# Performance work log

Hardware: AMD Instinct MI355X
Metric: run time of the kernel (lower is better)

The kernel has to match this reference:

```python
import jax, jax.numpy as jnp
import numpy as np

N_NODES = 20000
N_EDGES = 160000
B = 200      # num graphs (nodes per graph = 100)
T = 8        # num_tau
A = 10       # action_size
H = 4        # heads
D = 128      # out_channels
R = 4        # num_relations
NCOS = 64


def rgat(x, edge_index, edge_type, W, q, k, b):
    # W: [R, in, H*D]; q, k: [H*D, H]; b: [D]
    xw = jnp.einsum('ni,rio->nro', x, W)              # [N, R, H*D]
    src, dst = edge_index[0], edge_index[1]
    xj = xw[src, edge_type]                            # [E, H*D] gather by edge + relation
    xi = xw[dst, edge_type]                            # [E, H*D]
    alpha = jax.nn.leaky_relu(xi @ q + xj @ k, 0.2)    # [E, H]
    amax = jax.ops.segment_max(alpha, dst, num_segments=N_NODES)
    ex = jnp.exp(alpha - amax[dst])                    # segment softmax over dst
    denom = jax.ops.segment_sum(ex, dst, num_segments=N_NODES)
    a = ex / denom[dst]                                # [E, H]
    msg = (a[:, :, None] * xj.reshape(-1, H, D)).reshape(-1, H * D)
    agg = jax.ops.segment_sum(msg, dst, num_segments=N_NODES).reshape(-1, H, D)
    return agg.mean(axis=1) + b                        # concat=False -> mean over heads


def noisy_linear(z, w, bias, sw, sb, ew, eb):
    # torch convention: w [out, in]
    return z @ (w + sw * ew).T + (bias + sb * eb)


def setup_inputs():
    key = jax.random.key(0)
    ks = jax.random.split(key, 48)
    def rn(i, shape, scale=0.05):
        return jax.random.normal(ks[i], shape, dtype=jnp.float32) * scale
    SIG = 0.017
    inp = {
        'x': jax.random.normal(ks[0], (N_NODES, 2), dtype=jnp.float32),
        'edge_index': jax.random.randint(ks[1], (2, N_EDGES), 0, N_NODES, dtype=jnp.int32),
        'edge_type': jax.random.randint(ks[2], (N_EDGES,), 0, R, dtype=jnp.int32),
        'taus': jax.random.uniform(ks[3], (B, T, 1), dtype=jnp.float32),
        'W1': rn(4, (R, 2, H * D), 0.3), 'q1': rn(5, (H * D, H), 0.05), 'k1': rn(6, (H * D, H), 0.05), 'b1': rn(7, (D,)),
        'W2': rn(8, (R, D, H * D), 0.06), 'q2': rn(9, (H * D, H), 0.05), 'k2': rn(10, (H * D, H), 0.05), 'b2': rn(11, (D,)),
        'cos_w': rn(12, (D, NCOS), 0.1), 'cos_b': rn(13, (D,)),
        'ff1_w': rn(14, (D, D), 0.1), 'ff1_b': rn(15, (D,)),
        'ff1_sw': jnp.full((D, D), SIG, jnp.float32), 'ff1_sb': jnp.full((D,), SIG, jnp.float32),
        'ff1_ew': rn(16, (D, D), 1.0), 'ff1_eb': rn(17, (D,), 1.0),
        'ff2_w': rn(18, (D, D), 0.1), 'ff2_b': rn(19, (D,)),
        'ff2_sw': jnp.full((D, D), SIG, jnp.float32), 'ff2_sb': jnp.full((D,), SIG, jnp.float32),
        'ff2_ew': rn(20, (D, D), 1.0), 'ff2_eb': rn(21, (D,), 1.0),
        'adv_w': rn(22, (A, D), 0.1), 'adv_b': rn(23, (A,)),
        'adv_sw': jnp.full((A, D), SIG, jnp.float32), 'adv_sb': jnp.full((A,), SIG, jnp.float32),
        'adv_ew': rn(24, (A, D), 1.0), 'adv_eb': rn(25, (A,), 1.0),
        'val_w': rn(26, (1, D), 0.1), 'val_b': rn(27, (1,)),
        'val_sw': jnp.full((1, D), SIG, jnp.float32), 'val_sb': jnp.full((1,), SIG, jnp.float32),
        'val_ew': rn(28, (1, D), 1.0), 'val_eb': rn(29, (1,), 1.0),
    }
    return inp


def reference(x, edge_index, edge_type, taus,
              W1, q1, k1, b1, W2, q2, k2, b2, cos_w, cos_b,
              ff1_w, ff1_b, ff1_sw, ff1_sb, ff1_ew, ff1_eb,
              ff2_w, ff2_b, ff2_sw, ff2_sb, ff2_ew, ff2_eb,
              adv_w, adv_b, adv_sw, adv_sb, adv_ew, adv_eb,
              val_w, val_b, val_sw, val_sb, val_ew, val_eb):
    h = jax.nn.selu(rgat(x, edge_index, edge_type, W1, q1, k1, b1))
    h = jax.nn.selu(rgat(h, edge_index, edge_type, W2, q2, k2, b2))
    g = h.reshape(B, N_NODES // B, D).sum(axis=1)      # global_add_pool (block batch_idx)
    pis = jnp.pi * jnp.arange(1, NCOS + 1, dtype=jnp.float32)  # [NCOS]
    cos = jnp.cos(taus * pis)                           # [B, T, NCOS]
    cos_x = jax.nn.relu(cos @ cos_w.T + cos_b)          # [B, T, D]
    z = (g[:, None, :] * cos_x).reshape(B * T, D)
    z = jax.nn.selu(noisy_linear(z, ff1_w, ff1_b, ff1_sw, ff1_sb, ff1_ew, ff1_eb))
    z = jax.nn.selu(noisy_linear(z, ff2_w, ff2_b, ff2_sw, ff2_sb, ff2_ew, ff2_eb))
    adv = noisy_linear(z, adv_w, adv_b, adv_sw, adv_sb, adv_ew, adv_eb)   # [B*T, A]
    val = noisy_linear(z, val_w, val_b, val_sw, val_sb, val_ew, val_eb)   # [B*T, 1]
    out = val + adv - adv.mean(axis=1, keepdims=True)
    return out.reshape(B, T, A), taus
```

## Files before the change

kernel.cpp:

```cpp
#include <hip/hip_runtime.h>
#include <hip/hip_bf16.h>

constexpr long NN = 20000;
constexpr long NE = 160000;
constexpr long BB = 200;
constexpr long TT = 8;
constexpr long GN = 100;

constexpr long O_FLAG = 0;
constexpr long O_X    = 16;                 constexpr long N_X   = 40000;
constexpr long O_TAU  = O_X + N_X;          constexpr long N_TAU = 1600;
constexpr long O_W1   = O_TAU + N_TAU;      constexpr long N_W1  = 4096;
constexpr long O_Q1   = O_W1 + N_W1;        constexpr long N_Q   = 2048;
constexpr long O_K1   = O_Q1 + N_Q;
constexpr long O_B1   = O_K1 + N_Q;         constexpr long N_B   = 128;
constexpr long O_W2   = O_B1 + N_B;         constexpr long N_W2  = 262144;
constexpr long O_Q2   = O_W2 + N_W2;
constexpr long O_K2   = O_Q2 + N_Q;
constexpr long O_B2   = O_K2 + N_Q;
constexpr long O_CW   = O_B2 + N_B;         constexpr long N_CW  = 8192;
constexpr long O_CB   = O_CW + N_CW;
constexpr long O_F1W  = O_CB + N_B;         constexpr long N_FW  = 16384;
constexpr long O_F1B  = O_F1W + N_FW;
constexpr long O_F1SW = O_F1B + N_B;
constexpr long O_F1SB = O_F1SW + N_FW;
constexpr long O_F1EW = O_F1SB + N_B;
constexpr long O_F1EB = O_F1EW + N_FW;
constexpr long O_F2W  = O_F1EB + N_B;
constexpr long O_F2B  = O_F2W + N_FW;
constexpr long O_F2SW = O_F2B + N_B;
constexpr long O_F2SB = O_F2SW + N_FW;
constexpr long O_F2EW = O_F2SB + N_B;
constexpr long O_F2EB = O_F2EW + N_FW;
constexpr long O_AW   = O_F2EB + N_B;       constexpr long N_AW  = 1280;
constexpr long O_AB   = O_AW + N_AW;        constexpr long N_AB  = 16;
constexpr long O_ASW  = O_AB + N_AB;
constexpr long O_ASB  = O_ASW + N_AW;
constexpr long O_AEW  = O_ASB + N_AB;
constexpr long O_AEB  = O_AEW + N_AW;
constexpr long O_VW   = O_AEB + N_AB;       constexpr long N_VW  = 128;
constexpr long O_VB   = O_VW + N_VW;        constexpr long N_VB  = 16;
constexpr long O_VSW  = O_VB + N_VB;
constexpr long O_VSB  = O_VSW + N_VW;
constexpr long O_VEW  = O_VSB + N_VB;
constexpr long O_VEB  = O_VEW + N_VW;
constexpr long O_WQ1  = O_VEB + N_VB;
constexpr long O_WK1  = O_WQ1 + 32;
constexpr long O_WQ2  = O_WK1 + 32;
constexpr long O_WK2  = O_WQ2 + 2048;
constexpr long O_CF1W = O_WK2 + 2048;
constexpr long O_CF1B = O_CF1W + N_FW;
constexpr long O_CF2W = O_CF1B + N_B;
constexpr long O_CF2B = O_CF2W + N_FW;
constexpr long O_CAW  = O_CF2B + N_B;
constexpr long O_CAB  = O_CAW + N_AW;
constexpr long O_CVW  = O_CAB + N_AB;
constexpr long O_CVB  = O_CVW + N_VW;
constexpr long O_AL1  = O_CVB + N_VB;
constexpr long O_AL2  = O_AL1 + NE*4;
constexpr long O_H1   = O_AL2 + NE*4;
constexpr long O_H2   = O_H1 + NN*128;
constexpr long O_G    = O_H2 + NN*128;
constexpr long O_Z0   = O_G + BB*128;
constexpr long O_Z1   = O_Z0 + BB*TT*128;
constexpr long O_Z2   = O_Z1 + BB*TT*128;
constexpr long O_AGG1 = O_Z2 + BB*TT*128;
constexpr long O_DEG  = O_AGG1;
constexpr long O_CUR  = O_DEG + NN;
constexpr long O_ROWP = O_CUR + NN;
constexpr long O_PERM = O_ROWP + NN + 8;
constexpr long O_AGG2 = O_AGG1 + NN*128;
constexpr long O_DEN1 = O_AGG2 + NN*128;
constexpr long O_DEN2 = O_DEN1 + NN*4;
constexpr long O_AMAX1= O_DEN2 + NN*4;
constexpr long O_AMAX2= O_AMAX1 + NN*4;
constexpr long O_XW2  = O_AMAX2 + NN*4;
constexpr long O_END_TABLE = O_XW2 + (NN*4*512)/2;
constexpr long MPAD   = 20096;
constexpr long O_H1B  = O_END_TABLE;
constexpr long O_W2BT = O_H1B + (MPAD*128)/2;
constexpr long O_END2 = O_W2BT + (2048L*128)/2;
constexpr long O_AQ   = O_END2;
constexpr long O_AK   = O_AQ + NN*16;
constexpr long O_END3 = O_AK + NN*16;

constexpr int EMAX = 128;

#define DEVFN __device__ __forceinline__

typedef __attribute__((ext_vector_type(8))) short bf16x8;
typedef __attribute__((ext_vector_type(4))) float f32x4;
typedef __attribute__((ext_vector_type(4))) unsigned short u16x4;

DEVFN float selu_f(float x){ return 1.0507009873554805f * (x > 0.f ? x : 1.6732632423543772f * expm1f(x)); }
DEVFN float lrelu_f(float x){ return x >= 0.f ? x : 0.2f * x; }
DEVFN float bf2f(unsigned short u){ return __uint_as_float(((unsigned)u) << 16); }

__global__ void k_pre(const unsigned short* taus_u16, const int* ei, float* ws){
    if (blockIdx.x == 0){
        if (threadIdx.x == 0){
            int bf = 1;
            for (int i = 0; i < 128; i++) if (taus_u16[i] > 0x3F80u){ bf = 0; break; }
            ((int*)ws)[0] = bf;
        }
        return;
    }
    long e = (long)(blockIdx.x - 1)*blockDim.x + threadIdx.x;
    if (e >= NE) return;
    atomicAdd((int*)(ws + O_DEG) + ei[NE + e], 1);
}

__global__ void k_scan(float* ws){
    const int* deg = (const int*)(ws + O_DEG);
    int* rowp = (int*)(ws + O_ROWP);
    __shared__ int part[256];
    int tid = threadIdx.x;
    int base = tid * 79;
    int n = 0; if (base < NN) n = min(79, (int)NN - base);
    int s = 0;
    for (int i = 0; i < n; i++) s += deg[base + i];
    part[tid] = s;
    __syncthreads();
    if (tid == 0){
        int acc = 0;
        for (int i = 0; i < 256; i++){ int t = part[i]; part[i] = acc; acc += t; }
    }
    __syncthreads();
    int acc = part[tid];
    for (int i = 0; i < n; i++){ rowp[base + i] = acc; acc += deg[base + i]; }
    if (tid == 0) rowp[NN] = (int)NE;
}

struct ConvArgs { const void* src[38]; long off[38]; int n[38]; };

__global__ void k_conv_scatter(ConvArgs a, const int* ei, float* ws){
    int y = blockIdx.y;
    if (y == 38){
        long e = (long)blockIdx.x*blockDim.x + threadIdx.x;
        if (e >= NE) return;
        int dst = ei[NE + e];
        int pos = atomicAdd((int*)(ws + O_CUR) + dst, 1);
        ((int*)(ws + O_PERM))[((const int*)(ws + O_ROWP))[dst] + pos] = (int)e;
        return;
    }
    long off = a.off[y];
    if (off < 0) return;
    const void* s = a.src[y];
    int n = a.n[y];
    int bf = ((const int*)ws)[0];
    for (int i = blockIdx.x*blockDim.x + threadIdx.x; i < n; i += gridDim.x*blockDim.x){
        float v;
        if (bf){ unsigned short u = ((const unsigned short*)s)[i]; v = bf2f(u); }
        else   { v = ((const float*)s)[i]; }
        ws[off + i] = v;
    }
}

__global__ void k_prep(float* ws){
    int phase = blockIdx.y;
    int idx = blockIdx.x*blockDim.x + threadIdx.x;
    if (phase == 0){
        if (idx >= 4160) return;
        long wsrc, qsrc, dst; int ri, h;
        if (idx < 64){
            int t = idx & 31; h = t & 3; ri = t >> 2;
            wsrc = O_W1 + (long)ri*512;
            qsrc = (idx < 32) ? O_Q1 : O_K1;
            dst  = ((idx < 32) ? O_WQ1 : O_WK1) + t;
        } else {
            int t = (idx - 64) & 2047; h = t & 3; ri = t >> 2;
            wsrc = O_W2 + (long)ri*512;
            qsrc = (idx < 2112) ? O_Q2 : O_K2;
            dst  = ((idx < 2112) ? O_WQ2 : O_WK2) + t;
        }
        const float* W = ws + wsrc;
        const float* Q = ws + qsrc;
        float s = 0.f;
        for (int o = 0; o < 512; o++) s += W[o] * Q[o*4 + h];
        ws[dst] = s;
    } else if (phase == 1){
        const long tw[8] = {O_F1W,O_F2W,O_AW,O_VW, O_F1B,O_F2B,O_AB,O_VB};
        const long ts[8] = {O_F1SW,O_F2SW,O_ASW,O_VSW, O_F1SB,O_F2SB,O_ASB,O_VSB};
        const long te[8] = {O_F1EW,O_F2EW,O_AEW,O_VEW, O_F1EB,O_F2EB,O_AEB,O_VEB};
        const long td[8] = {O_CF1W,O_CF2W,O_CAW,O_CVW, O_CF1B,O_CF2B,O_CAB,O_CVB};
        const int  tn[8] = {16384,16384,1280,128, 128,128,10,1};
        const int  tb[8] = {0,16384,32768,34048, 34176,34304,34432,34442};
        int total = 34443;
        for (int i = idx; i < total; i += gridDim.x*blockDim.x){
            int t = 0;
            #pragma unroll
            for (int q = 1; q < 8; q++) if (i >= tb[q]) t = q;
            int j = i - tb[t];
            if (j < tn[t]) ws[td[t] + j] = ws[tw[t] + j] + ws[ts[t] + j]*ws[te[t] + j];
        }
    } else if (phase == 2){
        if (idx >= 262144) return;
        int np = idx & 2047, k = idx >> 11;
        int r = np >> 9, q = np & 511, d = q >> 2, h = q & 3;
        float v = ws[O_W2 + (long)r*65536 + (long)k*512 + h*128 + d];
        ((__hip_bfloat16*)(ws + O_W2BT))[(long)np*128 + k] = __float2bfloat16(v);
    } else {
        if (idx < 6144) ws[O_H1B + (20000L*128)/2 + idx] = 0.f;
    }
}

__global__ void k_node1(const int* ei, const int* et, float* ws){
    __shared__ float wqk[64];
    __shared__ float alc[EMAX][4];
    __shared__ float xsc[EMAX][2];
    __shared__ int   rtc[EMAX];
    __shared__ float sacc[4][4][2];
    __shared__ float den[4], amax[4];
    __shared__ float mred[2][4];
    int n = blockIdx.x, tid = threadIdx.x;
    const int* rowp = (const int*)(ws + O_ROWP);
    const int* perm = (const int*)(ws + O_PERM);
    int e0 = rowp[n], deg = rowp[n+1] - e0;
    if (tid < 64) wqk[tid] = ws[O_WQ1 + tid];
    if (tid < 32) ((float*)sacc)[tid] = 0.f;
    if (tid < 4) den[tid] = 0.f;
    float xd0 = ws[O_X + (long)n*2], xd1 = ws[O_X + (long)n*2 + 1];
    __syncthreads();
    float mx[4] = {-3.0e38f,-3.0e38f,-3.0e38f,-3.0e38f};
    for (int j0 = 0; j0 < deg; j0 += 128){
        int j = j0 + tid;
        if (j < deg){
            int e = perm[e0 + j];
            int src = ei[e], rt = et[e];
            float xs0 = ws[O_X + (long)src*2], xs1 = ws[O_X + (long)src*2 + 1];
            const float* Wq = wqk + rt*8;
            const float* Wk = wqk + 32 + rt*8;
            #pragma unroll
            for (int h = 0; h < 4; h++){
                float a = lrelu_f(xd0*Wq[h] + xd1*Wq[4+h] + xs0*Wk[h] + xs1*Wk[4+h]);
                if (j < EMAX) alc[j][h] = a;
                mx[h] = fmaxf(mx[h], a);
            }
            if (j < EMAX){ xsc[j][0] = xs0; xsc[j][1] = xs1; rtc[j] = rt; }
        }
    }
    #pragma unroll
    for (int off = 32; off > 0; off >>= 1)
        #pragma unroll
        for (int h = 0; h < 4; h++) mx[h] = fmaxf(mx[h], __shfl_xor(mx[h], off));
    if ((tid & 63) == 0)
        #pragma unroll
        for (int h = 0; h < 4; h++) mred[tid >> 6][h] = mx[h];
    __syncthreads();
    if (tid < 4) amax[tid] = fmaxf(mred[0][tid], mred[1][tid]);
    __syncthreads();
    for (int j0 = 0; j0 < deg; j0 += 128){
        int j = j0 + tid;
        if (j < deg){
            float al[4], xs0, xs1; int rt;
            if (j < EMAX){
                #pragma unroll
                for (int h = 0; h < 4; h++) al[h] = alc[j][h];
                xs0 = xsc[j][0]; xs1 = xsc[j][1]; rt = rtc[j];
            } else {
                int e = perm[e0 + j];
                int src = ei[e]; rt = et[e];
                xs0 = ws[O_X + (long)src*2]; xs1 = ws[O_X + (long)src*2 + 1];
                const float* Wq = wqk + rt*8;
                const float* Wk = wqk + 32 + rt*8;
                #pragma unroll
                for (int h = 0; h < 4; h++)
                    al[h] = lrelu_f(xd0*Wq[h] + xd1*Wq[4+h] + xs0*Wk[h] + xs1*Wk[4+h]);
            }
            #pragma unroll
            for (int h = 0; h < 4; h++){
                float ex = expf(al[h] - amax[h]);
                atomicAdd(&den[h], ex);
                atomicAdd(&sacc[rt][h][0], ex*xs0);
                atomicAdd(&sacc[rt][h][1], ex*xs1);
            }
        }
    }
    __syncthreads();
    int d = tid;
    float rden[4];
    #pragma unroll
    for (int h = 0; h < 4; h++) rden[h] = den[h] > 0.f ? 0.25f/den[h] : 0.f;
    float v = 0.f;
    #pragma unroll
    for (int r = 0; r < 4; r++)
        #pragma unroll
        for (int h = 0; h < 4; h++){
            float w0 = ws[O_W1 + r*1024 +        h*128 + d];
            float w1 = ws[O_W1 + r*1024 + 512  + h*128 + d];
            v += rden[h]*(w0*sacc[r][h][0] + w1*sacc[r][h][1]);
        }
    float out = selu_f(v + ws[O_B1 + d]);
    ((__hip_bfloat16*)(ws + O_H1B))[(long)n*128 + d] = __float2bfloat16(out);
}

__global__ void k_aqk(float* ws){
    __shared__ float wq[128*16];
    __shared__ float wk[128*16];
    __shared__ float hl[16][129];
    int tid = threadIdx.x;
    long nb = (long)blockIdx.x * 16;
    const unsigned short* h1b = (const unsigned short*)(ws + O_H1B);
    #pragma unroll
    for (int c = 0; c < 8; c++){
        int idx = tid + c*256;
        int i = idx >> 4, o = idx & 15;
        int r = o >> 2, h = o & 3;
        wq[i*16 + o] = ws[O_WQ2 + r*512 + i*4 + h];
        wk[i*16 + o] = ws[O_WK2 + r*512 + i*4 + h];
        hl[idx >> 7][idx & 127] = bf2f(h1b[nb*128 + idx]);
    }
    __syncthreads();
    int j = tid >> 4, o = tid & 15;
    float aq = 0.f, ak = 0.f;
    #pragma unroll 4
    for (int i = 0; i < 128; i++){
        float hv = hl[j][i];
        aq += hv * wq[i*16 + o];
        ak += hv * wk[i*16 + o];
    }
    ws[O_AQ + (nb + j)*16 + o] = aq;
    ws[O_AK + (nb + j)*16 + o] = ak;
}

__global__ void k_xw2_mfma(float* ws){
    __shared__ __align__(16) unsigned short Ash[128*128];
    __shared__ __align__(16) unsigned short Bsh[128*128];
    const unsigned short* h1b  = (const unsigned short*)(ws + O_H1B);
    const unsigned short* w2bt = (const unsigned short*)(ws + O_W2BT);
    long bm = (long)blockIdx.x * 128;
    long bn = (long)blockIdx.y * 128;
    int tid = threadIdx.x;
    char* Ac = (char*)Ash; char* Bc = (char*)Bsh;
    #pragma unroll
    for (int i = 0; i < 8; i++){
        int c = tid + i*256;
        int row = c >> 4, kb = (c & 15) * 16;
        int off = row*256 + (kb ^ ((row & 7) << 4));
        *(bf16x8*)(Ac + off) = *(const bf16x8*)&h1b [(bm + row)*128 + (c & 15)*8];
        *(bf16x8*)(Bc + off) = *(const bf16x8*)&w2bt[(bn + row)*128 + (c & 15)*8];
    }
    __syncthreads();
    int w = tid >> 6, lane = tid & 63;
    int wm = (w >> 1) * 64, wn = (w & 1) * 64;
    int r16 = lane & 15, kq = lane >> 4;
    f32x4 acc[4][4] = {};
    #pragma unroll
    for (int ks = 0; ks < 4; ks++){
        int kbyte = ks*64 + kq*16;
        bf16x8 a[4], b[4];
        #pragma unroll
        for (int m = 0; m < 4; m++){
            int row = wm + m*16 + r16;
            a[m] = *(const bf16x8*)(Ac + row*256 + (kbyte ^ ((row & 7) << 4)));
        }
        #pragma unroll
        for (int n = 0; n < 4; n++){
            int row = wn + n*16 + r16;
            b[n] = *(const bf16x8*)(Bc + row*256 + (kbyte ^ ((row & 7) << 4)));
        }
        #pragma unroll
        for (int m = 0; m < 4; m++)
            #pragma unroll
            for (int n = 0; n < 4; n++)
                acc[m][n] = __builtin_amdgcn_mfma_f32_16x16x32_bf16(a[m], b[n], acc[m][n], 0, 0, 0);
    }
    __hip_bfloat16* xb = (__hip_bfloat16*)(ws + O_XW2);
    #pragma unroll
    for (int m = 0; m < 4; m++){
        long gr0 = bm + wm + m*16 + kq*4;
        #pragma unroll
        for (int j = 0; j < 4; j++){
            long gr = gr0 + j;
            if (gr < NN){
                #pragma unroll
                for (int n = 0; n < 4; n++){
                    long gc = bn + wn + n*16 + r16;
                    xb[gr*2048 + gc] = __float2bfloat16(acc[m][n][j]);
                }
            }
        }
    }
}

__global__ void k_node2(const int* ei, const int* et, float* ws){
    __shared__ float aq[16];
    __shared__ float exc[EMAX][4];
    __shared__ int   esrt[EMAX];
    __shared__ float den[4], amax[4];
    __shared__ float mred[2][4];
    int n = blockIdx.x, tid = threadIdx.x;
    const int* rowp = (const int*)(ws + O_ROWP);
    const int* perm = (const int*)(ws + O_PERM);
    int e0 = rowp[n], deg = rowp[n+1] - e0;
    if (tid < 16) aq[tid] = ws[O_AQ + (long)n*16 + tid];
    if (tid < 4) den[tid] = 0.f;
    __syncthreads();
    float mx[4] = {-3.0e38f,-3.0e38f,-3.0e38f,-3.0e38f};
    for (int j0 = 0; j0 < deg; j0 += 128){
        int j = j0 + tid;
        if (j < deg){
            int e = perm[e0 + j];
            int src = ei[e], rt = et[e];
            float4 k4 = *(const float4*)&ws[O_AK + (long)src*16 + rt*4];
            float al0 = lrelu_f(aq[rt*4+0] + k4.x);
            float al1 = lrelu_f(aq[rt*4+1] + k4.y);
            float al2 = lrelu_f(aq[rt*4+2] + k4.z);
            float al3 = lrelu_f(aq[rt*4+3] + k4.w);
            if (j < EMAX){
                exc[j][0]=al0; exc[j][1]=al1; exc[j][2]=al2; exc[j][3]=al3;
                esrt[j] = src*4 + rt;
            }
            mx[0]=fmaxf(mx[0],al0); mx[1]=fmaxf(mx[1],al1);
            mx[2]=fmaxf(mx[2],al2); mx[3]=fmaxf(mx[3],al3);
        }
    }
    #pragma unroll
    for (int off = 32; off > 0; off >>= 1)
        #pragma unroll
        for (int h = 0; h < 4; h++) mx[h] = fmaxf(mx[h], __shfl_xor(mx[h], off));
    if ((tid & 63) == 0)
        #pragma unroll
        for (int h = 0; h < 4; h++) mred[tid >> 6][h] = mx[h];
    __syncthreads();
    if (tid < 4) amax[tid] = fmaxf(mred[0][tid], mred[1][tid]);
    __syncthreads();
    for (int j0 = 0; j0 < deg; j0 += 128){
        int j = j0 + tid;
        if (j < deg && j < EMAX){
            #pragma unroll
            for (int h = 0; h < 4; h++){
                float ex = expf(exc[j][h] - amax[h]);
                exc[j][h] = ex;
                atomicAdd(&den[h], ex);
            }
        } else if (j < deg){
            int e = perm[e0 + j];
            int src = ei[e], rt = et[e];
            float4 k4 = *(const float4*)&ws[O_AK + (long)src*16 + rt*4];
            float al[4] = {lrelu_f(aq[rt*4+0]+k4.x), lrelu_f(aq[rt*4+1]+k4.y),
                           lrelu_f(aq[rt*4+2]+k4.z), lrelu_f(aq[rt*4+3]+k4.w)};
            #pragma unroll
            for (int h = 0; h < 4; h++) atomicAdd(&den[h], expf(al[h]-amax[h]));
        }
    }
    __syncthreads();
    int d = tid;
    const unsigned short* xw2 = (const unsigned short*)(ws + O_XW2);
    float a0=0.f, a1=0.f, a2=0.f, a3=0.f;
    int mdeg = min(deg, EMAX);
    int j = 0;
    for (; j + 4 <= mdeg; j += 4){
        long s0 = esrt[j], s1 = esrt[j+1], s2 = esrt[j+2], s3 = esrt[j+3];
        u16x4 v0 = *(const u16x4*)(xw2 + s0*512 + (d << 2));
        u16x4 v1 = *(const u16x4*)(xw2 + s1*512 + (d << 2));
        u16x4 v2 = *(const u16x4*)(xw2 + s2*512 + (d << 2));
        u16x4 v3 = *(const u16x4*)(xw2 + s3*512 + (d << 2));
        a0 += exc[j  ][0]*bf2f(v0[0]); a1 += exc[j  ][1]*bf2f(v0[1]);
        a2 += exc[j  ][2]*bf2f(v0[2]); a3 += exc[j  ][3]*bf2f(v0[3]);
        a0 += exc[j+1][0]*bf2f(v1[0]); a1 += exc[j+1][1]*bf2f(v1[1]);
        a2 += exc[j+1][2]*bf2f(v1[2]); a3 += exc[j+1][3]*bf2f(v1[3]);
        a0 += exc[j+2][0]*bf2f(v2[0]); a1 += exc[j+2][1]*bf2f(v2[1]);
        a2 += exc[j+2][2]*bf2f(v2[2]); a3 += exc[j+2][3]*bf2f(v2[3]);
        a0 += exc[j+3][0]*bf2f(v3[0]); a1 += exc[j+3][1]*bf2f(v3[1]);
        a2 += exc[j+3][2]*bf2f(v3[2]); a3 += exc[j+3][3]*bf2f(v3[3]);
    }
    for (; j < mdeg; j++){
        long sr = esrt[j];
        u16x4 v = *(const u16x4*)(xw2 + sr*512 + (d << 2));
        a0 += exc[j][0]*bf2f(v[0]); a1 += exc[j][1]*bf2f(v[1]);
        a2 += exc[j][2]*bf2f(v[2]); a3 += exc[j][3]*bf2f(v[3]);
    }
    for (j = EMAX; j < deg; j++){
        int e = perm[e0 + j];
        int src = ei[e], rt = et[e];
        float4 k4 = *(const float4*)&ws[O_AK + (long)src*16 + rt*4];
        float e0h = expf(lrelu_f(aq[rt*4+0]+k4.x)-amax[0]);
        float e1h = expf(lrelu_f(aq[rt*4+1]+k4.y)-amax[1]);
        float e2h = expf(lrelu_f(aq[rt*4+2]+k4.z)-amax[2]);
        float e3h = expf(lrelu_f(aq[rt*4+3]+k4.w)-amax[3]);
        u16x4 v = *(const u16x4*)(xw2 + ((long)src*4 + rt)*512 + (d << 2));
        a0 += e0h*bf2f(v[0]); a1 += e1h*bf2f(v[1]);
        a2 += e2h*bf2f(v[2]); a3 += e3h*bf2f(v[3]);
    }
    float rd0 = den[0] > 0.f ? 0.25f/den[0] : 0.f;
    float rd1 = den[1] > 0.f ? 0.25f/den[1] : 0.f;
    float rd2 = den[2] > 0.f ? 0.25f/den[2] : 0.f;
    float rd3 = den[3] > 0.f ? 0.25f/den[3] : 0.f;
    float v = a0*rd0 + a1*rd1 + a2*rd2 + a3*rd3;
    ws[O_H2 + (long)n*128 + d] = selu_f(v + ws[O_B2 + d]);
}

__global__ void k_pool(float* ws){
    int b = blockIdx.x, d = threadIdx.x;
    float s = 0.f;
    for (int j = 0; j < GN; j++) s += ws[O_H2 + ((long)b*GN + j)*128 + d];
    ws[O_G + (long)b*128 + d] = s;
}

__global__ void k_tail(float* ws, void* d_out, const void* taus_raw){
    __shared__ float cs[64];
    __shared__ float row0[128], row1[128], row2[128];
    __shared__ float advs[12];
    int bt = blockIdx.x, t = threadIdx.x;
    int b = bt >> 3;
    if (t < 64){
        float tau = ws[O_TAU + bt];
        cs[t] = cosf(tau * (3.14159265358979323846f * (float)(t + 1)));
    }
    __syncthreads();
    {
        const float* cw = ws + O_CW + (long)t*64;
        float s = ws[O_CB + t];
        for (int c = 0; c < 64; c++) s += cs[c]*cw[c];
        s = fmaxf(s, 0.f);
        row0[t] = ws[O_G + (long)b*128 + t] * s;
    }
    __syncthreads();
    {
        const float* W = ws + O_CF1W + (long)t*128;
        float s = ws[O_CF1B + t];
        for (int i = 0; i < 128; i++) s += row0[i]*W[i];
        row1[t] = selu_f(s);
    }
    __syncthreads();
    {
        const float* W = ws + O_CF2W + (long)t*128;
        float s = ws[O_CF2B + t];
        for (int i = 0; i < 128; i++) s += row1[i]*W[i];
        row2[t] = selu_f(s);
    }
    __syncthreads();
    if (t < 11){
        const float* W = (t < 10) ? (ws + O_CAW + (long)t*128) : (ws + O_CVW);
        float s = (t < 10) ? ws[O_CAB + t] : ws[O_CVB];
        for (int i = 0; i < 128; i++) s += row2[i]*W[i];
        advs[t] = s;
    }
    __syncthreads();
    if (t == 0){
        float m = 0.f;
        #pragma unroll
        for (int a = 0; a < 10; a++) m += advs[a];
        m *= 0.1f;
        float val = advs[10];
        int bf = ((const int*)ws)[0];
        if (bf){
            __hip_bfloat16* out = (__hip_bfloat16*)d_out;
            for (int a = 0; a < 10; a++) out[(long)bt*10 + a] = __float2bfloat16(val + advs[a] - m);
            ((unsigned short*)d_out)[16000 + bt] = ((const unsigned short*)taus_raw)[bt];
        } else {
            float* out = (float*)d_out;
            for (int a = 0; a < 10; a++) out[(long)bt*10 + a] = val + advs[a] - m;
            out[16000 + bt] = ((const float*)taus_raw)[bt];
        }
    }
}

extern "C" void kernel_launch(void* const* d_in, const int* in_sizes, int n_in,
                              void* d_out, int out_size, void* d_ws, size_t ws_size,
                              hipStream_t stream){
    (void)in_sizes; (void)n_in; (void)out_size; (void)ws_size;
    float* ws = (float*)d_ws;
    const int* ei = (const int*)d_in[1];
    const int* et = (const int*)d_in[2];

    hipMemsetAsync(ws + O_DEG, 0, (size_t)(2*NN)*4, stream);

    k_pre<<<626, 256, 0, stream>>>((const unsigned short*)d_in[3], ei, ws);
    k_scan<<<1, 256, 0, stream>>>(ws);

    ConvArgs ca;
    static const long conv_o[38] = {
        O_X, -1, -1, O_TAU, O_W1, O_Q1, O_K1, O_B1, O_W2, O_Q2, O_K2, O_B2, O_CW, O_CB,
        O_F1W, O_F1B, O_F1SW, O_F1SB, O_F1EW, O_F1EB,
        O_F2W, O_F2B, O_F2SW, O_F2SB, O_F2EW, O_F2EB,
        O_AW, O_AB, O_ASW, O_ASB, O_AEW, O_AEB,
        O_VW, O_VB, O_VSW, O_VSB, O_VEW, O_VEB };
    static const int conv_n[38] = {
        40000, 0, 0, 1600, 4096, 2048, 2048, 128, 262144, 2048, 2048, 128, 8192, 128,
        16384, 128, 16384, 128, 16384, 128,
        16384, 128, 16384, 128, 16384, 128,
        1280, 10, 1280, 10, 1280, 10,
        128, 1, 128, 1, 128, 1 };
    for (int i = 0; i < 38; i++){ ca.src[i] = d_in[i]; ca.off[i] = conv_o[i]; ca.n[i] = conv_n[i]; }
    k_conv_scatter<<<dim3(625, 39), 256, 0, stream>>>(ca, ei, ws);

    k_prep<<<dim3(1024, 4), 256, 0, stream>>>(ws);

    k_node1<<<20000, 128, 0, stream>>>(ei, et, ws);

    k_xw2_mfma<<<dim3(157, 16), 256, 0, stream>>>(ws);
    k_aqk<<<1250, 256, 0, stream>>>(ws);
    k_node2<<<20000, 128, 0, stream>>>(ei, et, ws);

    k_pool<<<200, 128, 0, stream>>>(ws);
    k_tail<<<1600, 128, 0, stream>>>(ws, d_out, d_in[3]);
}
```

Baseline: 243.8 us.

## Map one wavefront per node in RGAT aggregation kernels with register reductions

Both node kernels now assign one 64-lane wavefront per destination node, packing four nodes into each 256-thread block, instead of one 128-thread block per node. Softmax max and sum use wave shuffles and per-lane register accumulators in place of shared-memory atomics and block barriers. Each lane now handles two output channels using wider 8-element bf16 loads. The goal is to cut block-launch, barrier and atomic overhead for nodes of small degree (about 8 on average). The cost is more register pressure from the 32 per-relation accumulators and more shuffle reductions in node1.

```diff
diff --git a/kernel.cpp b/kernel.cpp
--- a/kernel.cpp
+++ b/kernel.cpp
@@ -69,12 +69,7 @@
 constexpr long O_CUR  = O_DEG + NN;
 constexpr long O_ROWP = O_CUR + NN;
 constexpr long O_PERM = O_ROWP + NN + 8;
-constexpr long O_AGG2 = O_AGG1 + NN*128;
-constexpr long O_DEN1 = O_AGG2 + NN*128;
-constexpr long O_DEN2 = O_DEN1 + NN*4;
-constexpr long O_AMAX1= O_DEN2 + NN*4;
-constexpr long O_AMAX2= O_AMAX1 + NN*4;
-constexpr long O_XW2  = O_AMAX2 + NN*4;
+constexpr long O_XW2  = O_AGG1 + NN*128 + NN*128 + NN*16;
 constexpr long O_END_TABLE = O_XW2 + (NN*4*512)/2;
 constexpr long MPAD   = 20096;
 constexpr long O_H1B  = O_END_TABLE;
@@ -84,17 +79,29 @@
 constexpr long O_AK   = O_AQ + NN*16;
 constexpr long O_END3 = O_AK + NN*16;
 
-constexpr int EMAX = 128;
-
 #define DEVFN __device__ __forceinline__
 
 typedef __attribute__((ext_vector_type(8))) short bf16x8;
 typedef __attribute__((ext_vector_type(4))) float f32x4;
-typedef __attribute__((ext_vector_type(4))) unsigned short u16x4;
+typedef __attribute__((ext_vector_type(8))) unsigned short u16x8;
 
 DEVFN float selu_f(float x){ return 1.0507009873554805f * (x > 0.f ? x : 1.6732632423543772f * expm1f(x)); }
 DEVFN float lrelu_f(float x){ return x >= 0.f ? x : 0.2f * x; }
 DEVFN float bf2f(unsigned short u){ return __uint_as_float(((unsigned)u) << 16); }
+DEVFN float wred_max(float v){
+    #pragma unroll
+    for (int off = 32; off > 0; off >>= 1) v = fmaxf(v, __shfl_xor(v, off));
+    return v;
+}
+DEVFN float wred_sum(float v){
+    #pragma unroll
+    for (int off = 32; off > 0; off >>= 1) v += __shfl_xor(v, off);
+    return v;
+}
+DEVFN unsigned short f2bfu(float x){
+    __hip_bfloat16 b = __float2bfloat16(x);
+    return *(unsigned short*)&b;
+}
 
 __global__ void k_pre(const unsigned short* taus_u16, const int* ei, float* ws){
     if (blockIdx.x == 0){
@@ -204,94 +211,107 @@
     }
 }
 
-__global__ void k_node1(const int* ei, const int* et, float* ws){
-    __shared__ float wqk[64];
-    __shared__ float alc[EMAX][4];
-    __shared__ float xsc[EMAX][2];
-    __shared__ int   rtc[EMAX];
-    __shared__ float sacc[4][4][2];
-    __shared__ float den[4], amax[4];
-    __shared__ float mred[2][4];
-    int n = blockIdx.x, tid = threadIdx.x;
+__global__ __launch_bounds__(256) void k_node1(const int* ei, const int* et, float* ws){
+    int wid = threadIdx.x >> 6, lane = threadIdx.x & 63;
+    long n = (long)blockIdx.x*4 + wid;
     const int* rowp = (const int*)(ws + O_ROWP);
     const int* perm = (const int*)(ws + O_PERM);
     int e0 = rowp[n], deg = rowp[n+1] - e0;
-    if (tid < 64) wqk[tid] = ws[O_WQ1 + tid];
-    if (tid < 32) ((float*)sacc)[tid] = 0.f;
-    if (tid < 4) den[tid] = 0.f;
-    float xd0 = ws[O_X + (long)n*2], xd1 = ws[O_X + (long)n*2 + 1];
-    __syncthreads();
+    float xd0 = ws[O_X + n*2], xd1 = ws[O_X + n*2 + 1];
+    bool have = lane < deg;
+    float al[4], xs0 = 0.f, xs1 = 0.f; int rt0 = 0;
     float mx[4] = {-3.0e38f,-3.0e38f,-3.0e38f,-3.0e38f};
-    for (int j0 = 0; j0 < deg; j0 += 128){
-        int j = j0 + tid;
+    if (have){
+        int e = perm[e0 + lane]; int src = ei[e]; rt0 = et[e];
+        xs0 = ws[O_X + (long)src*2]; xs1 = ws[O_X + (long)src*2 + 1];
+        const float* Wq = ws + O_WQ1 + rt0*8;
+        const float* Wk = ws + O_WK1 + rt0*8;
+        #pragma unroll
+        for (int h = 0; h < 4; h++){
+            al[h] = lrelu_f(xd0*Wq[h] + xd1*Wq[4+h] + xs0*Wk[h] + xs1*Wk[4+h]);
+            mx[h] = al[h];
+        }
+    }
+    for (int j0 = 64; j0 < deg; j0 += 64){
+        int j = j0 + lane;
         if (j < deg){
-            int e = perm[e0 + j];
-            int src = ei[e], rt = et[e];
-            float xs0 = ws[O_X + (long)src*2], xs1 = ws[O_X + (long)src*2 + 1];
-            const float* Wq = wqk + rt*8;
-            const float* Wk = wqk + 32 + rt*8;
+            int e = perm[e0 + j]; int src = ei[e]; int rt = et[e];
+            float a0 = ws[O_X + (long)src*2], a1 = ws[O_X + (long)src*2 + 1];
+            const float* Wq = ws + O_WQ1 + rt*8;
+            const float* Wk = ws + O_WK1 + rt*8;
+            #pragma unroll
+            for (int h = 0; h < 4; h++)
+                mx[h] = fmaxf(mx[h], lrelu_f(xd0*Wq[h] + xd1*Wq[4+h] + a0*Wk[h] + a1*Wk[4+h]));
+        }
+    }
+    #pragma unroll
+    for (int h = 0; h < 4; h++) mx[h] = wred_max(mx[h]);
+    float s[4][4][2];
+    #pragma unroll
+    for (int r = 0; r < 4; r++)
+        #pragma unroll
+        for (int h = 0; h < 4; h++){ s[r][h][0] = 0.f; s[r][h][1] = 0.f; }
+    float den[4] = {0.f,0.f,0.f,0.f};
+    if (have){
+        #pragma unroll
+        for (int h = 0; h < 4; h++){
+            float ex = expf(al[h] - mx[h]);
+            den[h] += ex;
+            float c0 = ex*xs0, c1 = ex*xs1;
+            #pragma unroll
+            for (int r = 0; r < 4; r++){
+                if (r == rt0){ s[r][h][0] += c0; s[r][h][1] += c1; }
+            }
+        }
+    }
+    for (int j0 = 64; j0 < deg; j0 += 64){
+        int j = j0 + lane;
+        if (j < deg){
+            int e = perm[e0 + j]; int src = ei[e]; int rt = et[e];
+            float a0 = ws[O_X + (long)src*2], a1 = ws[O_X + (long)src*2 + 1];
+            const float* Wq = ws + O_WQ1 + rt*8;
+            const float* Wk = ws + O_WK1 + rt*8;
             #pragma unroll
             for (int h = 0; h < 4; h++){
-                float a = lrelu_f(xd0*Wq[h] + xd1*Wq[4+h] + xs0*Wk[h] + xs1*Wk[4+h]);
-                if (j < EMAX) alc[j][h] = a;
-                mx[h] = fmaxf(mx[h], a);
+                float a = lrelu_f(xd0*Wq[h] + xd1*Wq[4+h] + a0*Wk[h] + a1*Wk[4+h]);
+                float ex = expf(a - mx[h]);
+                den[h] += ex;
+                float c0 = ex*a0, c1 = ex*a1;
+                #pragma unroll
+                for (int r = 0; r < 4; r++){
+                    if (r == rt){ s[r][h][0] += c0; s[r][h][1] += c1; }
+                }
             }
-            if (j < EMAX){ xsc[j][0] = xs0; xsc[j][1] = xs1; rtc[j] = rt; }
-        }
-    }
-    #pragma unroll
-    for (int off = 32; off > 0; off >>= 1)
-        #pragma unroll
-        for (int h = 0; h < 4; h++) mx[h] = fmaxf(mx[h], __shfl_xor(mx[h], off));
-    if ((tid & 63) == 0)
-        #pragma unroll
-        for (int h = 0; h < 4; h++) mred[tid >> 6][h] = mx[h];
-    __syncthreads();
-    if (tid < 4) amax[tid] = fmaxf(mred[0][tid], mred[1][tid]);
-    __syncthreads();
-    for (int j0 = 0; j0 < deg; j0 += 128){
-        int j = j0 + tid;
-        if (j < deg){
-            float al[4], xs0, xs1; int rt;
-            if (j < EMAX){
-                #pragma unroll
-                for (int h = 0; h < 4; h++) al[h] = alc[j][h];
-                xs0 = xsc[j][0]; xs1 = xsc[j][1]; rt = rtc[j];
-            } else {
-                int e = perm[e0 + j];
-                int src = ei[e]; rt = et[e];
-                xs0 = ws[O_X + (long)src*2]; xs1 = ws[O_X + (long)src*2 + 1];
-                const float* Wq = wqk + rt*8;
-                const float* Wk = wqk + 32 + rt*8;
-                #pragma unroll
-                for (int h = 0; h < 4; h++)
-                    al[h] = lrelu_f(xd0*Wq[h] + xd1*Wq[4+h] + xs0*Wk[h] + xs1*Wk[4+h]);
-            }
-            #pragma unroll
-            for (int h = 0; h < 4; h++){
-                float ex = expf(al[h] - amax[h]);
-                atomicAdd(&den[h], ex);
-                atomicAdd(&sacc[rt][h][0], ex*xs0);
-                atomicAdd(&sacc[rt][h][1], ex*xs1);
-            }
-        }
-    }
-    __syncthreads();
-    int d = tid;
+        }
+    }
+    #pragma unroll
+    for (int h = 0; h < 4; h++) den[h] = wred_sum(den[h]);
+    #pragma unroll
+    for (int r = 0; r < 4; r++)
+        #pragma unroll
+        for (int h = 0; h < 4; h++){
+            s[r][h][0] = wred_sum(s[r][h][0]);
+            s[r][h][1] = wred_sum(s[r][h][1]);
+        }
     float rden[4];
     #pragma unroll
     for (int h = 0; h < 4; h++) rden[h] = den[h] > 0.f ? 0.25f/den[h] : 0.f;
-    float v = 0.f;
+    float v0 = 0.f, v1 = 0.f;
     #pragma unroll
     for (int r = 0; r < 4; r++)
         #pragma unroll
         for (int h = 0; h < 4; h++){
-            float w0 = ws[O_W1 + r*1024 +        h*128 + d];
-            float w1 = ws[O_W1 + r*1024 + 512  + h*128 + d];
-            v += rden[h]*(w0*sacc[r][h][0] + w1*sacc[r][h][1]);
-        }
-    float out = selu_f(v + ws[O_B1 + d]);
-    ((__hip_bfloat16*)(ws + O_H1B))[(long)n*128 + d] = __float2bfloat16(out);
+            float2 wa = *(const float2*)&ws[O_W1 + r*1024 +       h*128 + lane*2];
+            float2 wb = *(const float2*)&ws[O_W1 + r*1024 + 512 + h*128 + lane*2];
+            float t0 = s[r][h][0]*rden[h], t1 = s[r][h][1]*rden[h];
+            v0 += wa.x*t0 + wb.x*t1;
+            v1 += wa.y*t0 + wb.y*t1;
+        }
+    float2 b2 = *(const float2*)&ws[O_B1 + lane*2];
+    float o0 = selu_f(v0 + b2.x), o1 = selu_f(v1 + b2.y);
+    unsigned short* p = (unsigned short*)(ws + O_H1B) + n*128 + lane*2;
+    ushort2 pk; pk.x = f2bfu(o0); pk.y = f2bfu(o1);
+    *(ushort2*)p = pk;
 }
 
 __global__ void k_aqk(float* ws){
@@ -383,112 +403,116 @@
     }
 }
 
-__global__ void k_node2(const int* ei, const int* et, float* ws){
-    __shared__ float aq[16];
-    __shared__ float exc[EMAX][4];
-    __shared__ int   esrt[EMAX];
-    __shared__ float den[4], amax[4];
-    __shared__ float mred[2][4];
-    int n = blockIdx.x, tid = threadIdx.x;
+__global__ __launch_bounds__(256) void k_node2(const int* ei, const int* et, float* ws){
+    __shared__ float excs[4][64][4];
+    __shared__ int   esrts[4][64];
+    int wid = threadIdx.x >> 6, lane = threadIdx.x & 63;
+    long n = (long)blockIdx.x*4 + wid;
     const int* rowp = (const int*)(ws + O_ROWP);
     const int* perm = (const int*)(ws + O_PERM);
     int e0 = rowp[n], deg = rowp[n+1] - e0;
-    if (tid < 16) aq[tid] = ws[O_AQ + (long)n*16 + tid];
-    if (tid < 4) den[tid] = 0.f;
-    __syncthreads();
+    bool have = lane < deg;
+    float al[4]; int srt = 0;
     float mx[4] = {-3.0e38f,-3.0e38f,-3.0e38f,-3.0e38f};
-    for (int j0 = 0; j0 < deg; j0 += 128){
-        int j = j0 + tid;
+    if (have){
+        int e = perm[e0 + lane]; int src = ei[e]; int rt = et[e]; srt = src*4 + rt;
+        float4 q4 = *(const float4*)&ws[O_AQ + n*16 + rt*4];
+        float4 k4 = *(const float4*)&ws[O_AK + (long)src*16 + rt*4];
+        al[0] = lrelu_f(q4.x + k4.x); al[1] = lrelu_f(q4.y + k4.y);
+        al[2] = lrelu_f(q4.z + k4.z); al[3] = lrelu_f(q4.w + k4.w);
+        #pragma unroll
+        for (int h = 0; h < 4; h++) mx[h] = al[h];
+    }
+    for (int j0 = 64; j0 < deg; j0 += 64){
+        int j = j0 + lane;
         if (j < deg){
-            int e = perm[e0 + j];
-            int src = ei[e], rt = et[e];
+            int e = perm[e0 + j]; int src = ei[e]; int rt = et[e];
+            float4 q4 = *(const float4*)&ws[O_AQ + n*16 + rt*4];
             float4 k4 = *(const float4*)&ws[O_AK + (long)src*16 + rt*4];
-            float al0 = lrelu_f(aq[rt*4+0] + k4.x);
-            float al1 = lrelu_f(aq[rt*4+1] + k4.y);
-            float al2 = lrelu_f(aq[rt*4+2] + k4.z);
-            float al3 = lrelu_f(aq[rt*4+3] + k4.w);
-            if (j < EMAX){
-                exc[j][0]=al0; exc[j][1]=al1; exc[j][2]=al2; exc[j][3]=al3;
-                esrt[j] = src*4 + rt;
-            }
-            mx[0]=fmaxf(mx[0],al0); mx[1]=fmaxf(mx[1],al1);
-            mx[2]=fmaxf(mx[2],al2); mx[3]=fmaxf(mx[3],al3);
-        }
-    }
-    #pragma unroll
-    for (int off = 32; off > 0; off >>= 1)
-        #pragma unroll
-        for (int h = 0; h < 4; h++) mx[h] = fmaxf(mx[h], __shfl_xor(mx[h], off));
-    if ((tid & 63) == 0)
-        #pragma unroll
-        for (int h = 0; h < 4; h++) mred[tid >> 6][h] = mx[h];
-    __syncthreads();
-    if (tid < 4) amax[tid] = fmaxf(mred[0][tid], mred[1][tid]);
-    __syncthreads();
-    for (int j0 = 0; j0 < deg; j0 += 128){
-        int j = j0 + tid;
-        if (j < deg && j < EMAX){
-            #pragma unroll
-            for (int h = 0; h < 4; h++){
-                float ex = expf(exc[j][h] - amax[h]);
-                exc[j][h] = ex;
-                atomicAdd(&den[h], ex);
-            }
-        } else if (j < deg){
-            int e = perm[e0 + j];
-            int src = ei[e], rt = et[e];
+            mx[0] = fmaxf(mx[0], lrelu_f(q4.x + k4.x));
+            mx[1] = fmaxf(mx[1], lrelu_f(q4.y + k4.y));
+            mx[2] = fmaxf(mx[2], lrelu_f(q4.z + k4.z));
+            mx[3] = fmaxf(mx[3], lrelu_f(q4.w + k4.w));
+        }
+    }
+    #pragma unroll
+    for (int h = 0; h < 4; h++) mx[h] = wred_max(mx[h]);
+    float den[4] = {0.f,0.f,0.f,0.f};
+    if (have){
+        #pragma unroll
+        for (int h = 0; h < 4; h++){
+            float ex = expf(al[h] - mx[h]);
+            den[h] += ex;
+            excs[wid][lane][h] = ex;
+        }
+        esrts[wid][lane] = srt;
+    }
+    for (int j0 = 64; j0 < deg; j0 += 64){
+        int j = j0 + lane;
+        if (j < deg){
+            int e = perm[e0 + j]; int src = ei[e]; int rt = et[e];
+            float4 q4 = *(const float4*)&ws[O_AQ + n*16 + rt*4];
             float4 k4 = *(const float4*)&ws[O_AK + (long)src*16 + rt*4];
-            float al[4] = {lrelu_f(aq[rt*4+0]+k4.x), lrelu_f(aq[rt*4+1]+k4.y),
-                           lrelu_f(aq[rt*4+2]+k4.z), lrelu_f(aq[rt*4+3]+k4.w)};
-            #pragma unroll
-            for (int h = 0; h < 4; h++) atomicAdd(&den[h], expf(al[h]-amax[h]));
-        }
-    }
-    __syncthreads();
-    int d = tid;
+            den[0] += expf(lrelu_f(q4.x + k4.x) - mx[0]);
+            den[1] += expf(lrelu_f(q4.y + k4.y) - mx[1]);
+            den[2] += expf(lrelu_f(q4.z + k4.z) - mx[2]);
+            den[3] += expf(lrelu_f(q4.w + k4.w) - mx[3]);
+        }
+    }
+    #pragma unroll
+    for (int h = 0; h < 4; h++) den[h] = wred_sum(den[h]);
+    __syncthreads();
     const unsigned short* xw2 = (const unsigned short*)(ws + O_XW2);
-    float a0=0.f, a1=0.f, a2=0.f, a3=0.f;
-    int mdeg = min(deg, EMAX);
+    float a0[4] = {0.f,0.f,0.f,0.f}, a1[4] = {0.f,0.f,0.f,0.f};
+    int mdeg = min(deg, 64);
     int j = 0;
     for (; j + 4 <= mdeg; j += 4){
-        long s0 = esrt[j], s1 = esrt[j+1], s2 = esrt[j+2], s3 = esrt[j+3];
-        u16x4 v0 = *(const u16x4*)(xw2 + s0*512 + (d << 2));
-        u16x4 v1 = *(const u16x4*)(xw2 + s1*512 + (d << 2));
-        u16x4 v2 = *(const u16x4*)(xw2 + s2*512 + (d << 2));
-        u16x4 v3 = *(const u16x4*)(xw2 + s3*512 + (d << 2));
-        a0 += exc[j  ][0]*bf2f(v0[0]); a1 += exc[j  ][1]*bf2f(v0[1]);
-        a2 += exc[j  ][2]*bf2f(v0[2]); a3 += exc[j  ][3]*bf2f(v0[3]);
-        a0 += exc[j+1][0]*bf2f(v1[0]); a1 += exc[j+1][1]*bf2f(v1[1]);
-        a2 += exc[j+1][2]*bf2f(v1[2]); a3 += exc[j+1][3]*bf2f(v1[3]);
-        a0 += exc[j+2][0]*bf2f(v2[0]); a1 += exc[j+2][1]*bf2f(v2[1]);
-        a2 += exc[j+2][2]*bf2f(v2[2]); a3 += exc[j+2][3]*bf2f(v2[3]);
-        a0 += exc[j+3][0]*bf2f(v3[0]); a1 += exc[j+3][1]*bf2f(v3[1]);
-        a2 += exc[j+3][2]*bf2f(v3[2]); a3 += exc[j+3][3]*bf2f(v3[3]);
+        long s0 = esrts[wid][j], s1 = esrts[wid][j+1], s2 = esrts[wid][j+2], s3 = esrts[wid][j+3];
+        u16x8 v0 = *(const u16x8*)(xw2 + s0*512 + lane*8);
+        u16x8 v1 = *(const u16x8*)(xw2 + s1*512 + lane*8);
+        u16x8 v2 = *(const u16x8*)(xw2 + s2*512 + lane*8);
+        u16x8 v3 = *(const u16x8*)(xw2 + s3*512 + lane*8);
+        #pragma unroll
+        for (int h = 0; h < 4; h++){
+            a0[h] += excs[wid][j  ][h]*bf2f(v0[h]); a1[h] += excs[wid][j  ][h]*bf2f(v0[4+h]);
+            a0[h] += excs[wid][j+1][h]*bf2f(v1[h]); a1[h] += excs[wid][j+1][h]*bf2f(v1[4+h]);
+            a0[h] += excs[wid][j+2][h]*bf2f(v2[h]); a1[h] += excs[wid][j+2][h]*bf2f(v2[4+h]);
+            a0[h] += excs[wid][j+3][h]*bf2f(v3[h]); a1[h] += excs[wid][j+3][h]*bf2f(v3[4+h]);
+        }
     }
     for (; j < mdeg; j++){
-        long sr = esrt[j];
-        u16x4 v = *(const u16x4*)(xw2 + sr*512 + (d << 2));
-        a0 += exc[j][0]*bf2f(v[0]); a1 += exc[j][1]*bf2f(v[1]);
-        a2 += exc[j][2]*bf2f(v[2]); a3 += exc[j][3]*bf2f(v[3]);
-    }
-    for (j = EMAX; j < deg; j++){
-        int e = perm[e0 + j];
-        int src = ei[e], rt = et[e];
+        long sr = esrts[wid][j];
+        u16x8 v = *(const u16x8*)(xw2 + sr*512 + lane*8);
+        #pragma unroll
+        for (int h = 0; h < 4; h++){
+            a0[h] += excs[wid][j][h]*bf2f(v[h]);
+            a1[h] += excs[wid][j][h]*bf2f(v[4+h]);
+        }
+    }
+    for (j = 64; j < deg; j++){
+        int e = perm[e0 + j]; int src = ei[e]; int rt = et[e];
+        float4 q4 = *(const float4*)&ws[O_AQ + n*16 + rt*4];
         float4 k4 = *(const float4*)&ws[O_AK + (long)src*16 + rt*4];
-        float e0h = expf(lrelu_f(aq[rt*4+0]+k4.x)-amax[0]);
-        float e1h = expf(lrelu_f(aq[rt*4+1]+k4.y)-amax[1]);
-        float e2h = expf(lrelu_f(aq[rt*4+2]+k4.z)-amax[2]);
-        float e3h = expf(lrelu_f(aq[rt*4+3]+k4.w)-amax[3]);
-        u16x4 v = *(const u16x4*)(xw2 + ((long)src*4 + rt)*512 + (d << 2));
-        a0 += e0h*bf2f(v[0]); a1 += e1h*bf2f(v[1]);
-        a2 += e2h*bf2f(v[2]); a3 += e3h*bf2f(v[3]);
-    }
-    float rd0 = den[0] > 0.f ? 0.25f/den[0] : 0.f;
-    float rd1 = den[1] > 0.f ? 0.25f/den[1] : 0.f;
-    float rd2 = den[2] > 0.f ? 0.25f/den[2] : 0.f;
-    float rd3 = den[3] > 0.f ? 0.25f/den[3] : 0.f;
-    float v = a0*rd0 + a1*rd1 + a2*rd2 + a3*rd3;
-    ws[O_H2 + (long)n*128 + d] = selu_f(v + ws[O_B2 + d]);
+        float ex[4];
+        ex[0] = expf(lrelu_f(q4.x + k4.x) - mx[0]);
+        ex[1] = expf(lrelu_f(q4.y + k4.y) - mx[1]);
+        ex[2] = expf(lrelu_f(q4.z + k4.z) - mx[2]);
+        ex[3] = expf(lrelu_f(q4.w + k4.w) - mx[3]);
+        u16x8 v = *(const u16x8*)(xw2 + ((long)src*4 + rt)*512 + lane*8);
+        #pragma unroll
+        for (int h = 0; h < 4; h++){
+            a0[h] += ex[h]*bf2f(v[h]);
+            a1[h] += ex[h]*bf2f(v[4+h]);
+        }
+    }
+    float rd[4];
+    #pragma unroll
+    for (int h = 0; h < 4; h++) rd[h] = den[h] > 0.f ? 0.25f/den[h] : 0.f;
+    float o0 = a0[0]*rd[0] + a0[1]*rd[1] + a0[2]*rd[2] + a0[3]*rd[3];
+    float o1 = a1[0]*rd[0] + a1[1]*rd[1] + a1[2]*rd[2] + a1[3]*rd[3];
+    float2 b2 = *(const float2*)&ws[O_B2 + lane*2];
+    float2 outv; outv.x = selu_f(o0 + b2.x); outv.y = selu_f(o1 + b2.y);
+    *(float2*)&ws[O_H2 + n*128 + lane*2] = outv;
 }
 
 __global__ void k_pool(float* ws){
@@ -588,11 +612,11 @@
 
     k_prep<<<dim3(1024, 4), 256, 0, stream>>>(ws);
 
-    k_node1<<<20000, 128, 0, stream>>>(ei, et, ws);
+    k_node1<<<5000, 256, 0, stream>>>(ei, et, ws);
 
     k_xw2_mfma<<<dim3(157, 16), 256, 0, stream>>>(ws);
     k_aqk<<<1250, 256, 0, stream>>>(ws);
-    k_node2<<<20000, 128, 0, stream>>>(ei, et, ws);
+    k_node2<<<5000, 256, 0, stream>>>(ei, et, ws);
 
     k_pool<<<200, 128, 0, stream>>>(ws);
     k_tail<<<1600, 128, 0, stream>>>(ws, d_out, d_in[3]);
```

Measured after the change: 260.6 us. 1.07x slower.
